# Kernel optimization log

Hardware: AMD Instinct MI355X
Metric: run time of the kernel (lower is better)

Reference implementation:

```python
import jax, jax.numpy as jnp
import numpy as np

N, E, IN, H, D = 100000, 1600000, 128, 4, 64
NEG_SLOPE = 0.2
K_APPNP, ALPHA = 5, 0.5
BN_EPS = 1e-5


def setup_inputs() -> dict:
    key = jax.random.key(0)
    ks = jax.random.split(key, 12)
    return {
        'node_feats': jax.random.normal(ks[0], (N, IN), jnp.float32),
        'src': jax.random.randint(ks[1], (E,), 0, N, jnp.int32),
        'dst': jax.random.randint(ks[2], (E,), 0, N, jnp.int32),
        'W_fc': jax.random.normal(ks[3], (IN, H * D), jnp.float32) * (1.0 / np.sqrt(IN)),
        'attn_l': jax.random.normal(ks[4], (H, D), jnp.float32) * 0.1,
        'attn_r': jax.random.normal(ks[5], (H, D), jnp.float32) * 0.1,
        'W_res_gat': jax.random.normal(ks[6], (IN, H * D), jnp.float32) * (1.0 / np.sqrt(IN)),
        'gat_bias': jax.random.normal(ks[7], (H * D,), jnp.float32) * 0.01,
        'conv_w': jax.random.normal(ks[8], (1, H), jnp.float32) * 0.5,
        'conv_b': jax.random.normal(ks[9], (1,), jnp.float32) * 0.01,
        'W_res': jax.random.normal(ks[10], (D, IN), jnp.float32) * (1.0 / np.sqrt(IN)),
        'b_res': jax.random.normal(ks[11], (D,), jnp.float32) * 0.01,
        'gamma': jnp.ones((D,), jnp.float32),
        'beta': jnp.zeros((D,), jnp.float32),
    }


def reference(node_feats, src, dst, W_fc, attn_l, attn_r, W_res_gat, gat_bias,
              conv_w, conv_b, W_res, b_res, gamma, beta):
    # ---- GATConv (4 heads, residual, relu) ----
    feat = (node_feats @ W_fc).reshape(N, H, D)            # (N,H,D)
    el = jnp.einsum('nhd,hd->nh', feat, attn_l)            # (N,H)
    er = jnp.einsum('nhd,hd->nh', feat, attn_r)
    e = jax.nn.leaky_relu(el[src] + er[dst], NEG_SLOPE)    # (E,H)
    # edge softmax over incoming edges of each dst node
    emax = jax.ops.segment_max(e, dst, num_segments=N)     # (N,H)
    emax = jnp.where(jnp.isfinite(emax), emax, 0.0)
    ee = jnp.exp(e - emax[dst])                            # (E,H)
    denom = jax.ops.segment_sum(ee, dst, num_segments=N)   # (N,H)
    a = ee / jnp.maximum(denom[dst], 1e-9)                 # (E,H)
    msg = feat[src] * a[..., None]                         # (E,H,D)
    rst = jax.ops.segment_sum(msg, dst, num_segments=N)    # (N,H,D)
    resval = (node_feats @ W_res_gat).reshape(N, H, D)
    rst = jax.nn.relu(rst + resval + gat_bias.reshape(1, H, D))
    # ---- Conv1d (heads -> 1, kernel_size=1) then flatten ----
    h = jnp.einsum('nhd,oh->nod', rst, conv_w) + conv_b[None, :, None]
    h = h.reshape(N, D)
    # ---- APPNP (k=5, alpha=0.5), symmetric deg^{-1/2} norm (in-degree, clamp 1) ----
    deg = jax.ops.segment_sum(jnp.ones((E,), jnp.float32), dst, num_segments=N)
    norm = jnp.power(jnp.maximum(deg, 1.0), -0.5)[:, None]  # (N,1)
    h0 = h
    for _ in range(K_APPNP):
        h = jax.ops.segment_sum((h * norm)[src], dst, num_segments=N) * norm
        h = (1.0 - ALPHA) * h + ALPHA * h0
    # ---- residual linear + relu ----
    h = h + jax.nn.relu(node_feats @ W_res.T + b_res)
    # ---- BatchNorm1d (batch stats, affine) ----
    mu = h.mean(axis=0)
    var = h.var(axis=0)
    return (h - mu) * jax.lax.rsqrt(var + BN_EPS) * gamma + beta
```

## Files before the change

kernel.cpp:

```cpp
#include <hip/hip_runtime.h>
#include <math.h>

#define NN 100000
#define NE 1600000
#define NEG_SLOPE 0.2f
#define GB 98
#define GP 6250
#define SCR 2411u

typedef __attribute__((ext_vector_type(8))) short bf16x8;
typedef __attribute__((ext_vector_type(4))) float f32x4;
typedef __attribute__((ext_vector_type(2))) float f32x2;

__device__ __forceinline__ float b2f(unsigned short u) {
  union { unsigned u; float f; } c; c.u = ((unsigned)u) << 16; return c.f;
}
__device__ __forceinline__ unsigned short f2b(float x) {
  union { float f; unsigned u; } c; c.f = x;
  unsigned r = c.u + 0x7FFFu + ((c.u >> 16) & 1u);
  return (unsigned short)(r >> 16);
}
__device__ __forceinline__ void fma4(float4& acc, float s, const float4& b) {
  acc.x = fmaf(s, b.x, acc.x);
  acc.y = fmaf(s, b.y, acc.y);
  acc.z = fmaf(s, b.z, acc.z);
  acc.w = fmaf(s, b.w, acc.w);
}

__global__ __launch_bounds__(256) void k_zero(int* __restrict__ p, int nwords) {
  int i = blockIdx.x * 256 + threadIdx.x;
  if (i < nwords) p[i] = 0;
}

__global__ void k_zrow(unsigned short* __restrict__ a, unsigned short* __restrict__ b,
                       unsigned short* __restrict__ c) {
  int i = threadIdx.x;
  a[(size_t)NN * 64 + i] = 0;
  b[(size_t)NN * 64 + i] = 0;
  c[(size_t)NN * 64 + i] = 0;
}

__global__ __launch_bounds__(256) void k_cast(const float* __restrict__ A, unsigned short* __restrict__ Ab) {
  int i = blockIdx.x * 256 + threadIdx.x;
  int i4 = i * 4;
  if (i4 < NN * 128) {
    float4 v = *(const float4*)&A[i4];
    ushort4 o; o.x = f2b(v.x); o.y = f2b(v.y); o.z = f2b(v.z); o.w = f2b(v.w);
    *(ushort4*)&Ab[i4] = o;
  }
}

__global__ __launch_bounds__(256) void k_deg(const int* __restrict__ dst, int* __restrict__ deg) {
  int i = blockIdx.x * 256 + threadIdx.x;
  if (i < NE) atomicAdd(&deg[dst[i]], 1);
}

__global__ __launch_bounds__(256) void k_hist(const int* __restrict__ deg, int* __restrict__ bcount,
                                              int* __restrict__ bsum) {
  __shared__ int hist[64];
  __shared__ int red[256];
  int tid = threadIdx.x, blk = blockIdx.x;
  if (tid < 64) hist[tid] = 0;
  __syncthreads();
  int i0 = blk * 1024 + tid * 4;
  int s = 0;
#pragma unroll
  for (int r = 0; r < 4; ++r) {
    int i = i0 + r;
    if (i < NN) {
      int d = deg[i];
      s += d;
      atomicAdd(&hist[d < 63 ? d : 63], 1);
    }
  }
  red[tid] = s;
  __syncthreads();
  if (tid < 128) red[tid] += red[tid + 128];
  __syncthreads();
  if (tid < 64) {
    int v = red[tid] + red[tid + 64];
#pragma unroll
    for (int off = 32; off > 0; off >>= 1) v += __shfl_xor(v, off, 64);
    if (tid == 0) bsum[blk] = v;
    bcount[blk * 64 + tid] = hist[tid];
  }
}

__global__ void k_scan(int* __restrict__ bcount, const int* __restrict__ bsum,
                       int* __restrict__ dbase, int* __restrict__ bbase) {
  __shared__ int tot[64];
  int tid = threadIdx.x;
  {
    int s = 0;
#pragma unroll 7
    for (int blk = 0; blk < GB; ++blk) {
      int v = bcount[blk * 64 + tid];
      bcount[blk * 64 + tid] = s;
      s += v;
    }
    tot[tid] = s;
  }
  __syncthreads();
  if (tid == 0) {
    int base = 0;
    for (int b = 0; b < 64; ++b) { dbase[b] = base; base += tot[b]; }
  }
  if (tid == 1) {
    int s = 0;
#pragma unroll 7
    for (int blk = 0; blk < GB; ++blk) { bbase[blk] = s; s += bsum[blk]; }
  }
}

__global__ __launch_bounds__(256) void k_rows(const int* __restrict__ deg, const int* __restrict__ bcount,
                                              const int* __restrict__ dbase, const int* __restrict__ bbase,
                                              int* __restrict__ row_start, float* __restrict__ nrm,
                                              int* __restrict__ perm) {
  __shared__ int hist[64];
  __shared__ int sc[256];
  int tid = threadIdx.x, blk = blockIdx.x;
  if (tid < 64) hist[tid] = 0;
  int i0 = blk * 1024 + tid * 4;
  int d[4];
#pragma unroll
  for (int r = 0; r < 4; ++r) d[r] = (i0 + r < NN) ? deg[i0 + r] : 0;
  int ts = d[0] + d[1] + d[2] + d[3];
  sc[tid] = ts;
  __syncthreads();
  for (int off = 1; off < 256; off <<= 1) {
    int v = (tid >= off) ? sc[tid - off] : 0;
    __syncthreads();
    sc[tid] += v;
    __syncthreads();
  }
  int base = bbase[blk] + sc[tid] - ts;
#pragma unroll
  for (int r = 0; r < 4; ++r) {
    int i = i0 + r;
    if (i < NN) {
      row_start[i] = base;
      nrm[i] = rsqrtf(fmaxf((float)d[r], 1.0f));
      base += d[r];
      int b = d[r] < 63 ? d[r] : 63;
      int rank = atomicAdd(&hist[b], 1);
      perm[dbase[b] + bcount[blk * 64 + b] + rank] = i;
    }
  }
}

__global__ __launch_bounds__(256) void k_scatter(const int* __restrict__ src, const int* __restrict__ dst,
                                                 const int* __restrict__ row_start, int* __restrict__ cursor,
                                                 int* __restrict__ csr_src) {
  int i = blockIdx.x * 256 + threadIdx.x;
  if (i < NE) {
    int n = dst[i];
    int p = atomicAdd(&cursor[n], 1);
    csr_src[row_start[n] + p] = src[i];
  }
}

__global__ __launch_bounds__(256) void k_prepw(const float* __restrict__ W_fc, const float* __restrict__ al,
                                               const float* __restrict__ ar, float* __restrict__ w) {
  int o = blockIdx.x * 256 + threadIdx.x;
  if (o >= 1024) return;
  int side = o >> 9;
  int h = (o >> 7) & 3;
  int k = o & 127;
  const float* a = side ? ar : al;
  float s = 0.f;
  for (int d = 0; d < 64; ++d) s += W_fc[k * 256 + h * 64 + d] * a[h * 64 + d];
  w[(side * 4 + h) * 128 + k] = s;
}

__global__ __launch_bounds__(256) void k_elr2(const unsigned short* __restrict__ X, const float* __restrict__ w,
                                              float* __restrict__ el, float* __restrict__ er) {
  int n = blockIdx.x * 32 + (threadIdx.x >> 3);
  int p = threadIdx.x & 7;
  if (n >= NN) return;
  const uint4* xr = (const uint4*)(X + (size_t)n * 128);
  const float4* wr = (const float4*)(w + p * 128);
  float s = 0.f;
#pragma unroll
  for (int i = 0; i < 16; ++i) {
    uint4 x = xr[i];
    float4 w0 = wr[2 * i], w1 = wr[2 * i + 1];
    s += __uint_as_float(x.x << 16) * w0.x + __uint_as_float(x.x & 0xFFFF0000u) * w0.y
       + __uint_as_float(x.y << 16) * w0.z + __uint_as_float(x.y & 0xFFFF0000u) * w0.w
       + __uint_as_float(x.z << 16) * w1.x + __uint_as_float(x.z & 0xFFFF0000u) * w1.y
       + __uint_as_float(x.w << 16) * w1.z + __uint_as_float(x.w & 0xFFFF0000u) * w1.w;
  }
  if (p < 4) el[n * 4 + p] = s;
  else er[n * 4 + (p - 4)] = s;
}

__global__ __launch_bounds__(256) void k_prepB(const float* __restrict__ W_fc, const float* __restrict__ W_rg,
                                               unsigned short* __restrict__ Bp) {
  int y = blockIdx.y;
  const float* Bsrc = (y >> 1) ? W_rg : W_fc;
  int colbase = (y & 1) * 128;
  for (int e = blockIdx.x * 256 + threadIdx.x; e < 16384; e += 2048) {
    int n = e & 127, k = e >> 7;
    int p = colbase + n;
    int d = p >> 2, hh = p & 3;
    float v = Bsrc[k * 256 + hh * 64 + d];
    int nt = n >> 4, nn = n & 15, kt = k >> 5, quad = (k >> 3) & 3, j = k & 7;
    Bp[(size_t)y * 16384 + ((kt * 8 + nt) * 64 + quad * 16 + nn) * 8 + j] = f2b(v);
  }
}

__global__ __launch_bounds__(256) void k_gemm_mfma(const unsigned short* __restrict__ Abf,
                                                   const unsigned short* __restrict__ Bp,
                                                   unsigned* __restrict__ feat8u,
                                                   unsigned short* __restrict__ resval2) {
  __shared__ unsigned short Al[128 * 136];
  __shared__ unsigned short Bl[8192];
  int tid = threadIdx.x;
  int half = blockIdx.y >> 1;
  int colbase = (blockIdx.y & 1) * 128;
  int row0 = blockIdx.x * 128;
#pragma unroll
  for (int i = 0; i < 8; ++i) {
    int c = tid + i * 256;
    int row = c >> 4, part = c & 15;
    int gr = row0 + row; if (gr > NN - 1) gr = NN - 1;
    *(uint4*)&Al[row * 136 + part * 8] = *(const uint4*)&Abf[(size_t)gr * 128 + part * 8];
  }
  {
    const uint4* srcb = (const uint4*)(Bp + (size_t)blockIdx.y * 16384);
    uint4* dst4 = (uint4*)Bl;
#pragma unroll
    for (int i = 0; i < 4; ++i) dst4[tid + i * 256] = srcb[tid + i * 256];
  }
  __syncthreads();
  int w = tid >> 6, lane = tid & 63;
  int quad = lane >> 4, l16 = lane & 15;
  f32x4 acc[8][2];
#pragma unroll
  for (int rt = 0; rt < 8; ++rt)
#pragma unroll
    for (int c = 0; c < 2; ++c) acc[rt][c] = (f32x4){0.f, 0.f, 0.f, 0.f};
#pragma unroll
  for (int kh = 0; kh < 2; ++kh) {
    if (kh == 1) {
      __syncthreads();
      const uint4* srcb = (const uint4*)(Bp + (size_t)blockIdx.y * 16384 + 8192);
      uint4* dst4 = (uint4*)Bl;
#pragma unroll
      for (int i = 0; i < 4; ++i) dst4[tid + i * 256] = srcb[tid + i * 256];
      __syncthreads();
    }
#pragma unroll
    for (int ktl = 0; ktl < 2; ++ktl) {
      int kt = kh * 2 + ktl;
      bf16x8 b0 = *(const bf16x8*)&Bl[((ktl * 8 + w * 2 + 0) * 64 + lane) * 8];
      bf16x8 b1 = *(const bf16x8*)&Bl[((ktl * 8 + w * 2 + 1) * 64 + lane) * 8];
      int kb = kt * 32 + quad * 8;
#pragma unroll
      for (int rt = 0; rt < 8; ++rt) {
        bf16x8 a = *(const bf16x8*)&Al[(rt * 16 + l16) * 136 + kb];
        acc[rt][0] = __builtin_amdgcn_mfma_f32_16x16x32_bf16(b0, a, acc[rt][0], 0, 0, 0);
        acc[rt][1] = __builtin_amdgcn_mfma_f32_16x16x32_bf16(b1, a, acc[rt][1], 0, 0, 0);
      }
    }
  }
  __syncthreads();
  if (half == 0) {
    unsigned* Cl = (unsigned*)Al;
#pragma unroll
    for (int rt = 0; rt < 8; ++rt)
#pragma unroll
      for (int c = 0; c < 2; ++c) {
        int pk = __builtin_amdgcn_cvt_pk_fp8_f32(acc[rt][c][0], acc[rt][c][1], 0, false);
        pk = __builtin_amdgcn_cvt_pk_fp8_f32(acc[rt][c][2], acc[rt][c][3], pk, true);
        Cl[(rt * 16 + l16) * 36 + (w * 2 + c) * 4 + quad] = (unsigned)pk;
      }
    __syncthreads();
#pragma unroll
    for (int i = 0; i < 4; ++i) {
      int c = tid + i * 256;
      int row = c >> 3, wp = c & 7;
      int m = row0 + row;
      if (m < NN)
        *(uint4*)&feat8u[(size_t)m * 64 + (colbase >> 2) + wp * 4] = *(const uint4*)&Cl[row * 36 + wp * 4];
    }
  } else {
#pragma unroll
    for (int rt = 0; rt < 8; ++rt)
#pragma unroll
      for (int c = 0; c < 2; ++c) {
        int col = (w * 2 + c) * 16 + quad * 4;
        ushort4 o;
        o.x = f2b(acc[rt][c][0]); o.y = f2b(acc[rt][c][1]);
        o.z = f2b(acc[rt][c][2]); o.w = f2b(acc[rt][c][3]);
        *(ushort4*)&Al[(rt * 16 + l16) * 136 + col] = o;
      }
    __syncthreads();
#pragma unroll
    for (int i = 0; i < 8; ++i) {
      int c = tid + i * 256;
      int row = c >> 4, part = c & 15;
      int m = row0 + row;
      if (m < NN)
        *(uint4*)&resval2[(size_t)m * 256 + colbase + part * 8] = *(const uint4*)&Al[row * 136 + part * 8];
    }
  }
}

__global__ __launch_bounds__(256) void k_gemm_nt_bias_relu(const float* __restrict__ A, const float* __restrict__ B,
                                                           const float* __restrict__ bias, float* __restrict__ C) {
  __shared__ float Bl[128][68];
  for (int idx = threadIdx.x; idx < 64 * 128; idx += 256) {
    int d = idx >> 7, k = idx & 127;
    Bl[k][d] = B[d * 128 + k];
  }
  __syncthreads();
  int tx = threadIdx.x & 15, ty = threadIdx.x >> 4;
  int row0 = blockIdx.x * 64 + ty * 4;
  const float* ap[4];
#pragma unroll
  for (int r = 0; r < 4; ++r) ap[r] = A + (size_t)min(row0 + r, NN - 1) * 128;
  float4 acc[4];
#pragma unroll
  for (int r = 0; r < 4; ++r) acc[r] = make_float4(0.f, 0.f, 0.f, 0.f);
#pragma unroll 2
  for (int k0 = 0; k0 < 128; k0 += 4) {
    float4 b0 = *(const float4*)&Bl[k0][tx * 4];
    float4 b1 = *(const float4*)&Bl[k0 + 1][tx * 4];
    float4 b2 = *(const float4*)&Bl[k0 + 2][tx * 4];
    float4 b3 = *(const float4*)&Bl[k0 + 3][tx * 4];
#pragma unroll
    for (int r = 0; r < 4; ++r) {
      float4 a = *(const float4*)(ap[r] + k0);
      fma4(acc[r], a.x, b0); fma4(acc[r], a.y, b1);
      fma4(acc[r], a.z, b2); fma4(acc[r], a.w, b3);
    }
  }
  float4 bv = *(const float4*)&bias[tx * 4];
#pragma unroll
  for (int r = 0; r < 4; ++r) {
    int row = row0 + r;
    if (row < NN) {
      float4 v;
      v.x = fmaxf(acc[r].x + bv.x, 0.f);
      v.y = fmaxf(acc[r].y + bv.y, 0.f);
      v.z = fmaxf(acc[r].z + bv.z, 0.f);
      v.w = fmaxf(acc[r].w + bv.w, 0.f);
      *(float4*)&C[(size_t)row * 64 + tx * 4] = v;
    }
  }
}

__global__ __launch_bounds__(256) void k_gat(const int* __restrict__ perm, const int* __restrict__ row_start,
                                             const int* __restrict__ deg, const int* __restrict__ csr_src,
                                             const float* __restrict__ el, const float* __restrict__ er,
                                             const unsigned* __restrict__ feat8u,
                                             const unsigned short* __restrict__ resval2,
                                             const float* __restrict__ gat_bias, const float* __restrict__ conv_w,
                                             const float* __restrict__ conv_b, const float* __restrict__ nrm,
                                             float* __restrict__ h0, unsigned short* __restrict__ hs0o) {
  __shared__ int s_src[4][16][4];
  __shared__ float s_x[4][16][4][4];
  int wid = threadIdx.x >> 6, lane = threadIdx.x & 63;
  int g = lane >> 4, k = lane & 15;
  int chunk = (int)(((unsigned)blockIdx.x * SCR) % (unsigned)GP);
  int n = perm[chunk * 16 + wid * 4 + g];
  int s0 = row_start[n], cnt = deg[n];
  float4 er4 = *(const float4*)&er[n * 4];
  unsigned koff = (unsigned)(k << 4);
  f32x2 a01[4], a23[4];
#pragma unroll
  for (int i = 0; i < 4; ++i) { a01[i] = (f32x2){0.f, 0.f}; a23[i] = (f32x2){0.f, 0.f}; }
  f32x2 den01 = (f32x2){0.f, 0.f}, den23 = (f32x2){0.f, 0.f};
  int cm = cnt;
  cm = max(cm, __shfl_xor(cm, 16, 64));
  cm = max(cm, __shfl_xor(cm, 32, 64));
  for (int base = 0; base < cm; base += 16) {
    int j = base + k;
    int s = 0;
    float x0 = 0.f, x1 = 0.f, x2 = 0.f, x3 = 0.f;
    if (j < cnt) {
      s = csr_src[s0 + j];
      float4 el4 = *(const float4*)&el[s * 4];
      float e0 = el4.x + er4.x; e0 = (e0 > 0.f) ? e0 : NEG_SLOPE * e0;
      float e1 = el4.y + er4.y; e1 = (e1 > 0.f) ? e1 : NEG_SLOPE * e1;
      float e2 = el4.z + er4.z; e2 = (e2 > 0.f) ? e2 : NEG_SLOPE * e2;
      float e3 = el4.w + er4.w; e3 = (e3 > 0.f) ? e3 : NEG_SLOPE * e3;
      x0 = __expf(e0); x1 = __expf(e1); x2 = __expf(e2); x3 = __expf(e3);
      den01 += (f32x2){x0, x1}; den23 += (f32x2){x2, x3};
    }
    s_src[wid][k][g] = s;
    *(float4*)&s_x[wid][k][g][0] = make_float4(x0, x1, x2, x3);
    int tm = cm - base; if (tm > 16) tm = 16;
    int tm2 = (tm + 1) & ~1;
    for (int t = 0; t < tm2; t += 2) {
      int sa = s_src[wid][t][g];
      int sb = s_src[wid][t + 1][g];
      uint4 fa = *(const uint4*)((const char*)feat8u + (((unsigned)sa << 8) + koff));
      uint4 fb = *(const uint4*)((const char*)feat8u + (((unsigned)sb << 8) + koff));
      float4 xa = *(const float4*)&s_x[wid][t][g][0];
      float4 xb = *(const float4*)&s_x[wid][t + 1][g][0];
      {
        f32x2 x01 = (f32x2){xa.x, xa.y}, x23 = (f32x2){xa.z, xa.w};
        f32x2 lo, hi;
        lo = __builtin_amdgcn_cvt_pk_f32_fp8((int)fa.x, false);
        hi = __builtin_amdgcn_cvt_pk_f32_fp8((int)fa.x, true);
        a01[0] += x01 * lo; a23[0] += x23 * hi;
        lo = __builtin_amdgcn_cvt_pk_f32_fp8((int)fa.y, false);
        hi = __builtin_amdgcn_cvt_pk_f32_fp8((int)fa.y, true);
        a01[1] += x01 * lo; a23[1] += x23 * hi;
        lo = __builtin_amdgcn_cvt_pk_f32_fp8((int)fa.z, false);
        hi = __builtin_amdgcn_cvt_pk_f32_fp8((int)fa.z, true);
        a01[2] += x01 * lo; a23[2] += x23 * hi;
        lo = __builtin_amdgcn_cvt_pk_f32_fp8((int)fa.w, false);
        hi = __builtin_amdgcn_cvt_pk_f32_fp8((int)fa.w, true);
        a01[3] += x01 * lo; a23[3] += x23 * hi;
      }
      {
        f32x2 x01 = (f32x2){xb.x, xb.y}, x23 = (f32x2){xb.z, xb.w};
        f32x2 lo, hi;
        lo = __builtin_amdgcn_cvt_pk_f32_fp8((int)fb.x, false);
        hi = __builtin_amdgcn_cvt_pk_f32_fp8((int)fb.x, true);
        a01[0] += x01 * lo; a23[0] += x23 * hi;
        lo = __builtin_amdgcn_cvt_pk_f32_fp8((int)fb.y, false);
        hi = __builtin_amdgcn_cvt_pk_f32_fp8((int)fb.y, true);
        a01[1] += x01 * lo; a23[1] += x23 * hi;
        lo = __builtin_amdgcn_cvt_pk_f32_fp8((int)fb.z, false);
        hi = __builtin_amdgcn_cvt_pk_f32_fp8((int)fb.z, true);
        a01[2] += x01 * lo; a23[2] += x23 * hi;
        lo = __builtin_amdgcn_cvt_pk_f32_fp8((int)fb.w, false);
        hi = __builtin_amdgcn_cvt_pk_f32_fp8((int)fb.w, true);
        a01[3] += x01 * lo; a23[3] += x23 * hi;
      }
    }
  }
#pragma unroll
  for (int off = 1; off < 16; off <<= 1) {
    den01[0] += __shfl_xor(den01[0], off, 64);
    den01[1] += __shfl_xor(den01[1], off, 64);
    den23[0] += __shfl_xor(den23[0], off, 64);
    den23[1] += __shfl_xor(den23[1], off, 64);
  }
  float i0 = 1.f / fmaxf(den01[0], 1e-9f);
  float i1 = 1.f / fmaxf(den01[1], 1e-9f);
  float i2 = 1.f / fmaxf(den23[0], 1e-9f);
  float i3 = 1.f / fmaxf(den23[1], 1e-9f);
  uint4 rv0 = *(const uint4*)&resval2[(size_t)n * 256 + (k << 4)];
  uint4 rv1 = *(const uint4*)&resval2[(size_t)n * 256 + (k << 4) + 8];
  unsigned short c[16];
  *(uint4*)&c[0] = rv0; *(uint4*)&c[8] = rv1;
  int d0 = k << 2;
  float4 b0 = *(const float4*)&gat_bias[d0];
  float4 b1 = *(const float4*)&gat_bias[64 + d0];
  float4 b2 = *(const float4*)&gat_bias[128 + d0];
  float4 b3 = *(const float4*)&gat_bias[192 + d0];
  float bh0[4] = {b0.x, b0.y, b0.z, b0.w};
  float bh1[4] = {b1.x, b1.y, b1.z, b1.w};
  float bh2[4] = {b2.x, b2.y, b2.z, b2.w};
  float bh3[4] = {b3.x, b3.y, b3.z, b3.w};
  float cb = conv_b[0];
  float cw0 = conv_w[0], cw1 = conv_w[1], cw2 = conv_w[2], cw3 = conv_w[3];
  float hm[4];
#pragma unroll
  for (int i = 0; i < 4; ++i) {
    float t_, hmv = cb;
    t_ = fmaf(a01[i][0], i0, b2f(c[4 * i + 0]) + bh0[i]); t_ = fmaxf(t_, 0.f); hmv = fmaf(cw0, t_, hmv);
    t_ = fmaf(a01[i][1], i1, b2f(c[4 * i + 1]) + bh1[i]); t_ = fmaxf(t_, 0.f); hmv = fmaf(cw1, t_, hmv);
    t_ = fmaf(a23[i][0], i2, b2f(c[4 * i + 2]) + bh2[i]); t_ = fmaxf(t_, 0.f); hmv = fmaf(cw2, t_, hmv);
    t_ = fmaf(a23[i][1], i3, b2f(c[4 * i + 3]) + bh3[i]); t_ = fmaxf(t_, 0.f); hmv = fmaf(cw3, t_, hmv);
    hm[i] = hmv;
  }
  float nn_ = nrm[n];
  size_t o = (size_t)n * 64 + d0;
  *(float4*)&h0[o] = make_float4(hm[0], hm[1], hm[2], hm[3]);
  ushort4 hs;
  hs.x = f2b(hm[0] * nn_); hs.y = f2b(hm[1] * nn_);
  hs.z = f2b(hm[2] * nn_); hs.w = f2b(hm[3] * nn_);
  *(ushort4*)&hs0o[o] = hs;
}

__device__ __forceinline__ void gather4(const int* __restrict__ perm, const int* __restrict__ row_start,
                                        const int* __restrict__ deg, const int* __restrict__ csr_src,
                                        const unsigned short* __restrict__ hs_in,
                                        int wid, int lane, int& n, int& k, float (&a)[4]) {
  __shared__ int s_src[4][16][4];
  int g = lane >> 4; k = lane & 15;
  int chunk = (int)(((unsigned)blockIdx.x * SCR) % (unsigned)GP);
  n = perm[chunk * 16 + wid * 4 + g];
  int s0 = row_start[n], cnt = deg[n];
  unsigned koff = (unsigned)(k << 3);
  a[0] = 0.f; a[1] = 0.f; a[2] = 0.f; a[3] = 0.f;
  int cm = cnt;
  cm = max(cm, __shfl_xor(cm, 16, 64));
  cm = max(cm, __shfl_xor(cm, 32, 64));
  for (int base = 0; base < cm; base += 16) {
    int j = base + k;
    s_src[wid][k][g] = (j < cnt) ? csr_src[s0 + j] : NN;
    int tm = cm - base; if (tm > 16) tm = 16;
    int tm4 = (tm + 3) & ~3;
    for (int t = 0; t < tm4; t += 4) {
      int sa = s_src[wid][t][g];
      int sb = s_src[wid][t + 1][g];
      int sc2 = s_src[wid][t + 2][g];
      int sd = s_src[wid][t + 3][g];
      uint2 ua = *(const uint2*)((const char*)hs_in + (((unsigned)sa << 7) + koff));
      uint2 ub = *(const uint2*)((const char*)hs_in + (((unsigned)sb << 7) + koff));
      uint2 uc = *(const uint2*)((const char*)hs_in + (((unsigned)sc2 << 7) + koff));
      uint2 ud = *(const uint2*)((const char*)hs_in + (((unsigned)sd << 7) + koff));
      a[0] += __uint_as_float(ua.x << 16) + __uint_as_float(ub.x << 16);
      a[1] += __uint_as_float(ua.x & 0xFFFF0000u) + __uint_as_float(ub.x & 0xFFFF0000u);
      a[2] += __uint_as_float(ua.y << 16) + __uint_as_float(ub.y << 16);
      a[3] += __uint_as_float(ua.y & 0xFFFF0000u) + __uint_as_float(ub.y & 0xFFFF0000u);
      a[0] += __uint_as_float(uc.x << 16) + __uint_as_float(ud.x << 16);
      a[1] += __uint_as_float(uc.x & 0xFFFF0000u) + __uint_as_float(ud.x & 0xFFFF0000u);
      a[2] += __uint_as_float(uc.y << 16) + __uint_as_float(ud.y << 16);
      a[3] += __uint_as_float(uc.y & 0xFFFF0000u) + __uint_as_float(ud.y & 0xFFFF0000u);
    }
  }
}

__global__ __launch_bounds__(256) void k_gather_mid(const int* __restrict__ perm, const int* __restrict__ row_start,
                                                    const int* __restrict__ deg, const int* __restrict__ csr_src,
                                                    const unsigned short* __restrict__ hs_in,
                                                    const float* __restrict__ nrm,
                                                    const unsigned short* __restrict__ hs0,
                                                    unsigned short* __restrict__ hs_out) {
  int wid = threadIdx.x >> 6, lane = threadIdx.x & 63;
  int n, k; float a[4];
  gather4(perm, row_start, deg, csr_src, hs_in, wid, lane, n, k, a);
  size_t o = (size_t)n * 64 + (k << 2);
  float nn_ = nrm[n];
  float hnn = 0.5f * nn_ * nn_;
  uint2 z = *(const uint2*)&hs0[o];
  ushort4 ov;
  ov.x = f2b(fmaf(hnn, a[0], 0.5f * __uint_as_float(z.x << 16)));
  ov.y = f2b(fmaf(hnn, a[1], 0.5f * __uint_as_float(z.x & 0xFFFF0000u)));
  ov.z = f2b(fmaf(hnn, a[2], 0.5f * __uint_as_float(z.y << 16)));
  ov.w = f2b(fmaf(hnn, a[3], 0.5f * __uint_as_float(z.y & 0xFFFF0000u)));
  *(ushort4*)&hs_out[o] = ov;
}

__global__ __launch_bounds__(256) void k_gather_last(const int* __restrict__ perm, const int* __restrict__ row_start,
                                                     const int* __restrict__ deg, const int* __restrict__ csr_src,
                                                     const unsigned short* __restrict__ hs_in,
                                                     const float* __restrict__ nrm,
                                                     const float* __restrict__ res2,
                                                     float* h0io) {
  int wid = threadIdx.x >> 6, lane = threadIdx.x & 63;
  int n, k; float a[4];
  gather4(perm, row_start, deg, csr_src, hs_in, wid, lane, n, k, a);
  size_t o = (size_t)n * 64 + (k << 2);
  float nn_ = nrm[n];
  float hn = 0.5f * nn_;
  float4 h4 = *(const float4*)&h0io[o];
  float4 r4 = *(const float4*)&res2[o];
  float4 v;
  v.x = fmaf(hn, a[0], 0.5f * h4.x) + r4.x;
  v.y = fmaf(hn, a[1], 0.5f * h4.y) + r4.y;
  v.z = fmaf(hn, a[2], 0.5f * h4.z) + r4.z;
  v.w = fmaf(hn, a[3], 0.5f * h4.w) + r4.w;
  *(float4*)&h0io[o] = v;
}

__global__ __launch_bounds__(256) void k_finred(const float* __restrict__ hfin, float* __restrict__ bn) {
  __shared__ float s1[256], s2[256];
  int d = threadIdx.x & 63;
  int rb = blockIdx.x * 64;
  float sum = 0.f, sq = 0.f;
  for (int r = threadIdx.x >> 6; r < 64; r += 4) {
    int n = rb + r;
    if (n < NN) {
      float v = hfin[(size_t)n * 64 + d];
      sum += v; sq += v * v;
    }
  }
  s1[threadIdx.x] = sum; s2[threadIdx.x] = sq;
  __syncthreads();
  if (threadIdx.x < 128) { s1[threadIdx.x] += s1[threadIdx.x + 128]; s2[threadIdx.x] += s2[threadIdx.x + 128]; }
  __syncthreads();
  if (threadIdx.x < 64) {
    atomicAdd(&bn[d], s1[threadIdx.x] + s1[threadIdx.x + 64]);
    atomicAdd(&bn[64 + d], s2[threadIdx.x] + s2[threadIdx.x + 64]);
  }
}

__global__ void k_bnstats(const float* __restrict__ bn, const float* __restrict__ gamma,
                          const float* __restrict__ beta, float* __restrict__ bns) {
  int d = threadIdx.x;
  float mu = bn[d] * (1.0f / NN);
  float var = fmaxf(bn[64 + d] * (1.0f / NN) - mu * mu, 0.f);
  float sc = rsqrtf(var + 1e-5f) * gamma[d];
  bns[d] = sc;
  bns[64 + d] = beta[d] - mu * sc;
}

__global__ __launch_bounds__(256) void k_bnapply(const float* __restrict__ h, const float* __restrict__ bns,
                                                 float* __restrict__ out) {
  int i = blockIdx.x * 256 + threadIdx.x;
  if (i < NN * 64) {
    int d = i & 63;
    out[i] = fmaf(h[i], bns[d], bns[64 + d]);
  }
}

extern "C" void kernel_launch(void* const* d_in, const int* in_sizes, int n_in,
                              void* d_out, int out_size, void* d_ws, size_t ws_size,
                              hipStream_t stream) {
  const float* node_feats = (const float*)d_in[0];
  const int* src = (const int*)d_in[1];
  const int* dst = (const int*)d_in[2];
  const float* W_fc = (const float*)d_in[3];
  const float* attn_l = (const float*)d_in[4];
  const float* attn_r = (const float*)d_in[5];
  const float* W_res_gat = (const float*)d_in[6];
  const float* gat_bias = (const float*)d_in[7];
  const float* conv_w = (const float*)d_in[8];
  const float* conv_b = (const float*)d_in[9];
  const float* W_res = (const float*)d_in[10];
  const float* b_res = (const float*)d_in[11];
  const float* gamma = (const float*)d_in[12];
  const float* beta = (const float*)d_in[13];
  float* out = (float*)d_out;

  char* base = (char*)d_ws;
  size_t off = 0;
  auto alloc = [&](size_t bytes) -> char* {
    char* p = base + off;
    off = (off + bytes + 255) & ~(size_t)255;
    return p;
  };
  unsigned* feat8u        = (unsigned*)alloc((size_t)NN * 256);
  unsigned short* resval2 = (unsigned short*)alloc((size_t)NN * 256 * 2);
  float* res2             = (float*)resval2;
  float* el               = (float*)alloc((size_t)NN * 4 * 4);
  float* er               = (float*)alloc((size_t)NN * 4 * 4);
  float* h0               = (float*)alloc((size_t)NN * 64 * 4);
  unsigned short* Abf     = (unsigned short*)h0;
  unsigned short* hs0     = (unsigned short*)alloc((size_t)(NN + 1) * 64 * 2);
  unsigned short* hsA     = (unsigned short*)alloc((size_t)(NN + 1) * 64 * 2);
  unsigned short* hsB     = (unsigned short*)alloc((size_t)(NN + 1) * 64 * 2);
  int* csr_src            = (int*)alloc((size_t)NE * 4);
  float* nrm              = (float*)alloc((size_t)NN * 4);
  int* row_start          = (int*)alloc((size_t)NN * 4);
  int* perm               = (int*)alloc((size_t)NN * 4);
  int* bcount             = (int*)alloc((size_t)GB * 64 * 4);
  int* bsum               = (int*)alloc((size_t)GB * 4);
  int* bbase              = (int*)alloc((size_t)GB * 4);
  int* dbase              = (int*)alloc(64 * 4);
  unsigned short* Bpacked = (unsigned short*)alloc((size_t)4 * 16384 * 2);
  float* w_elr            = (float*)alloc((size_t)8 * 128 * 4);
  size_t zoff = off;
  int* deg                = (int*)alloc((size_t)NN * 4);
  int* cursor             = (int*)alloc((size_t)NN * 4);
  float* bn               = (float*)alloc(256 * 4);
  float* hfin             = h0;

  int zwords = (int)((off - zoff) / 4);
  int gE = (NE + 255) / 256;
  int gM = (NN + 63) / 64;
  int gV = (NN * 64 + 255) / 256;

  k_zero<<<(zwords + 255) / 256, 256, 0, stream>>>((int*)(base + zoff), zwords);
  k_zrow<<<1, 64, 0, stream>>>(hs0, hsA, hsB);
  k_deg<<<gE, 256, 0, stream>>>(dst, deg);
  k_hist<<<GB, 256, 0, stream>>>(deg, bcount, bsum);
  k_scan<<<1, 64, 0, stream>>>(bcount, bsum, dbase, bbase);
  k_rows<<<GB, 256, 0, stream>>>(deg, bcount, dbase, bbase, row_start, nrm, perm);
  k_scatter<<<gE, 256, 0, stream>>>(src, dst, row_start, cursor, csr_src);

  k_cast<<<(NN * 128 / 4 + 255) / 256, 256, 0, stream>>>(node_feats, Abf);
  k_prepB<<<dim3(8, 4), 256, 0, stream>>>(W_fc, W_res_gat, Bpacked);
  k_prepw<<<4, 256, 0, stream>>>(W_fc, attn_l, attn_r, w_elr);
  k_gemm_mfma<<<dim3((NN + 127) / 128, 4), 256, 0, stream>>>(Abf, Bpacked, feat8u, resval2);

  k_elr2<<<(NN + 31) / 32, 256, 0, stream>>>(Abf, w_elr, el, er);
  k_gat<<<GP, 256, 0, stream>>>(perm, row_start, deg, csr_src, el, er, feat8u, resval2,
                                gat_bias, conv_w, conv_b, nrm, h0, hs0);

  k_gemm_nt_bias_relu<<<gM, 256, 0, stream>>>(node_feats, W_res, b_res, res2);

  k_gather_mid<<<GP, 256, 0, stream>>>(perm, row_start, deg, csr_src, hs0, nrm, hs0, hsA);
  k_gather_mid<<<GP, 256, 0, stream>>>(perm, row_start, deg, csr_src, hsA, nrm, hs0, hsB);
  k_gather_mid<<<GP, 256, 0, stream>>>(perm, row_start, deg, csr_src, hsB, nrm, hs0, hsA);
  k_gather_mid<<<GP, 256, 0, stream>>>(perm, row_start, deg, csr_src, hsA, nrm, hs0, hsB);
  k_gather_last<<<GP, 256, 0, stream>>>(perm, row_start, deg, csr_src, hsB, nrm, res2, hfin);

  k_finred<<<gM, 256, 0, stream>>>(hfin, bn);
  k_bnstats<<<1, 64, 0, stream>>>(bn, gamma, beta, bn + 128);
  k_bnapply<<<gV, 256, 0, stream>>>(hfin, bn + 128, out);
}
```

Baseline: 729.0 us.

## Slice APPNP feature table into 8 column planes to shrink gather working set

Stores the bf16 scaled node features as 8 separate column slices of 16 bytes per node. Each APPNP block now handles one slice for 128 nodes, with two lanes per node, so each pass gathers from a table about 1.6MB in size that fits in cache. The GAT kernel no longer writes the fp32 h0. The last APPNP step instead rebuilds h0 from the bf16 scaled copy by dividing out the norm, which avoids one fp32 read and write but adds bf16 rounding error to h0. The trade-off is 8x more blocks, each re-reading CSR indices and degrees, and serial per-edge loads with less memory-level parallelism.

```diff
diff --git a/kernel.cpp b/kernel.cpp
--- a/kernel.cpp
+++ b/kernel.cpp
@@ -7,6 +7,9 @@
 #define GB 98
 #define GP 6250
 #define SCR 2411u
+#define NCH 782
+#define SCR2 389u
+#define SST ((NN + 1) * 8)
 
 typedef __attribute__((ext_vector_type(8))) short bf16x8;
 typedef __attribute__((ext_vector_type(4))) float f32x4;
@@ -35,9 +38,8 @@
 __global__ void k_zrow(unsigned short* __restrict__ a, unsigned short* __restrict__ b,
                        unsigned short* __restrict__ c) {
   int i = threadIdx.x;
-  a[(size_t)NN * 64 + i] = 0;
-  b[(size_t)NN * 64 + i] = 0;
-  c[(size_t)NN * 64 + i] = 0;
+  int idx = (i >> 3) * SST + NN * 8 + (i & 7);
+  a[idx] = 0; b[idx] = 0; c[idx] = 0;
 }
 
 __global__ __launch_bounds__(256) void k_cast(const float* __restrict__ A, unsigned short* __restrict__ Ab) {
@@ -357,7 +359,7 @@
                                              const unsigned short* __restrict__ resval2,
                                              const float* __restrict__ gat_bias, const float* __restrict__ conv_w,
                                              const float* __restrict__ conv_b, const float* __restrict__ nrm,
-                                             float* __restrict__ h0, unsigned short* __restrict__ hs0o) {
+                                             unsigned short* __restrict__ hs0o) {
   __shared__ int s_src[4][16][4];
   __shared__ float s_x[4][16][4][4];
   int wid = threadIdx.x >> 6, lane = threadIdx.x & 63;
@@ -470,95 +472,95 @@
     hm[i] = hmv;
   }
   float nn_ = nrm[n];
-  size_t o = (size_t)n * 64 + d0;
-  *(float4*)&h0[o] = make_float4(hm[0], hm[1], hm[2], hm[3]);
   ushort4 hs;
   hs.x = f2b(hm[0] * nn_); hs.y = f2b(hm[1] * nn_);
   hs.z = f2b(hm[2] * nn_); hs.w = f2b(hm[3] * nn_);
-  *(ushort4*)&hs0o[o] = hs;
-}
-
-__device__ __forceinline__ void gather4(const int* __restrict__ perm, const int* __restrict__ row_start,
-                                        const int* __restrict__ deg, const int* __restrict__ csr_src,
-                                        const unsigned short* __restrict__ hs_in,
-                                        int wid, int lane, int& n, int& k, float (&a)[4]) {
-  __shared__ int s_src[4][16][4];
-  int g = lane >> 4; k = lane & 15;
-  int chunk = (int)(((unsigned)blockIdx.x * SCR) % (unsigned)GP);
-  n = perm[chunk * 16 + wid * 4 + g];
-  int s0 = row_start[n], cnt = deg[n];
-  unsigned koff = (unsigned)(k << 3);
+  *(ushort4*)&hs0o[(size_t)(k >> 1) * SST + n * 8 + ((k & 1) << 2)] = hs;
+}
+
+__device__ __forceinline__ void appnp_core(const int* __restrict__ perm, const int* __restrict__ row_start,
+                                           const int* __restrict__ deg, const int* __restrict__ csr_src,
+                                           const unsigned short* __restrict__ hs_in,
+                                           int& s, int& n, int& h, bool& valid, float (&a)[4]) {
+  __shared__ int s_src[4][16][32];
+  int tid = threadIdx.x;
+  int wid = tid >> 6, lane = tid & 63;
+  int m = lane >> 1; h = lane & 1;
+  s = blockIdx.x & 7;
+  int chunk = (int)((((unsigned)blockIdx.x >> 3) * SCR2) % (unsigned)NCH);
+  int idx = chunk * 128 + wid * 32 + m;
+  valid = idx < NN;
+  n = perm[valid ? idx : NN - 1];
+  int cnt = valid ? deg[n] : 0;
+  int s0 = row_start[n];
+  const char* tbl = (const char*)(hs_in + (size_t)s * SST);
   a[0] = 0.f; a[1] = 0.f; a[2] = 0.f; a[3] = 0.f;
   int cm = cnt;
-  cm = max(cm, __shfl_xor(cm, 16, 64));
-  cm = max(cm, __shfl_xor(cm, 32, 64));
+#pragma unroll
+  for (int off = 1; off < 64; off <<= 1) cm = max(cm, __shfl_xor(cm, off, 64));
   for (int base = 0; base < cm; base += 16) {
-    int j = base + k;
-    s_src[wid][k][g] = (j < cnt) ? csr_src[s0 + j] : NN;
+#pragma unroll
+    for (int q = 0; q < 8; ++q) {
+      int slot = h * 8 + q;
+      int j = base + slot;
+      s_src[wid][slot][m] = (j < cnt) ? csr_src[s0 + j] : NN;
+    }
     int tm = cm - base; if (tm > 16) tm = 16;
-    int tm4 = (tm + 3) & ~3;
-    for (int t = 0; t < tm4; t += 4) {
-      int sa = s_src[wid][t][g];
-      int sb = s_src[wid][t + 1][g];
-      int sc2 = s_src[wid][t + 2][g];
-      int sd = s_src[wid][t + 3][g];
-      uint2 ua = *(const uint2*)((const char*)hs_in + (((unsigned)sa << 7) + koff));
-      uint2 ub = *(const uint2*)((const char*)hs_in + (((unsigned)sb << 7) + koff));
-      uint2 uc = *(const uint2*)((const char*)hs_in + (((unsigned)sc2 << 7) + koff));
-      uint2 ud = *(const uint2*)((const char*)hs_in + (((unsigned)sd << 7) + koff));
-      a[0] += __uint_as_float(ua.x << 16) + __uint_as_float(ub.x << 16);
-      a[1] += __uint_as_float(ua.x & 0xFFFF0000u) + __uint_as_float(ub.x & 0xFFFF0000u);
-      a[2] += __uint_as_float(ua.y << 16) + __uint_as_float(ub.y << 16);
-      a[3] += __uint_as_float(ua.y & 0xFFFF0000u) + __uint_as_float(ub.y & 0xFFFF0000u);
-      a[0] += __uint_as_float(uc.x << 16) + __uint_as_float(ud.x << 16);
-      a[1] += __uint_as_float(uc.x & 0xFFFF0000u) + __uint_as_float(ud.x & 0xFFFF0000u);
-      a[2] += __uint_as_float(uc.y << 16) + __uint_as_float(ud.y << 16);
-      a[3] += __uint_as_float(uc.y & 0xFFFF0000u) + __uint_as_float(ud.y & 0xFFFF0000u);
-    }
-  }
-}
-
-__global__ __launch_bounds__(256) void k_gather_mid(const int* __restrict__ perm, const int* __restrict__ row_start,
+    for (int t = 0; t < tm; ++t) {
+      int sidx = s_src[wid][t][m];
+      uint2 u = *(const uint2*)(tbl + (((unsigned)sidx << 4) + (h << 3)));
+      a[0] += __uint_as_float(u.x << 16);
+      a[1] += __uint_as_float(u.x & 0xFFFF0000u);
+      a[2] += __uint_as_float(u.y << 16);
+      a[3] += __uint_as_float(u.y & 0xFFFF0000u);
+    }
+  }
+}
+
+__global__ __launch_bounds__(256) void k_appnp_mid(const int* __restrict__ perm, const int* __restrict__ row_start,
+                                                   const int* __restrict__ deg, const int* __restrict__ csr_src,
+                                                   const unsigned short* __restrict__ hs_in,
+                                                   const float* __restrict__ nrm,
+                                                   const unsigned short* __restrict__ hs0,
+                                                   unsigned short* __restrict__ hs_out) {
+  int s, n, h; bool valid; float a[4];
+  appnp_core(perm, row_start, deg, csr_src, hs_in, s, n, h, valid, a);
+  if (valid) {
+    float nn_ = nrm[n];
+    float hnn = 0.5f * nn_ * nn_;
+    uint2 z = *(const uint2*)((const char*)(hs0 + (size_t)s * SST) + ((n << 4) + (h << 3)));
+    ushort4 ov;
+    ov.x = f2b(fmaf(hnn, a[0], 0.5f * __uint_as_float(z.x << 16)));
+    ov.y = f2b(fmaf(hnn, a[1], 0.5f * __uint_as_float(z.x & 0xFFFF0000u)));
+    ov.z = f2b(fmaf(hnn, a[2], 0.5f * __uint_as_float(z.y << 16)));
+    ov.w = f2b(fmaf(hnn, a[3], 0.5f * __uint_as_float(z.y & 0xFFFF0000u)));
+    *(ushort4*)&hs_out[(size_t)s * SST + n * 8 + (h << 2)] = ov;
+  }
+}
+
+__global__ __launch_bounds__(256) void k_appnp_last(const int* __restrict__ perm, const int* __restrict__ row_start,
                                                     const int* __restrict__ deg, const int* __restrict__ csr_src,
                                                     const unsigned short* __restrict__ hs_in,
                                                     const float* __restrict__ nrm,
                                                     const unsigned short* __restrict__ hs0,
-                                                    unsigned short* __restrict__ hs_out) {
-  int wid = threadIdx.x >> 6, lane = threadIdx.x & 63;
-  int n, k; float a[4];
-  gather4(perm, row_start, deg, csr_src, hs_in, wid, lane, n, k, a);
-  size_t o = (size_t)n * 64 + (k << 2);
-  float nn_ = nrm[n];
-  float hnn = 0.5f * nn_ * nn_;
-  uint2 z = *(const uint2*)&hs0[o];
-  ushort4 ov;
-  ov.x = f2b(fmaf(hnn, a[0], 0.5f * __uint_as_float(z.x << 16)));
-  ov.y = f2b(fmaf(hnn, a[1], 0.5f * __uint_as_float(z.x & 0xFFFF0000u)));
-  ov.z = f2b(fmaf(hnn, a[2], 0.5f * __uint_as_float(z.y << 16)));
-  ov.w = f2b(fmaf(hnn, a[3], 0.5f * __uint_as_float(z.y & 0xFFFF0000u)));
-  *(ushort4*)&hs_out[o] = ov;
-}
-
-__global__ __launch_bounds__(256) void k_gather_last(const int* __restrict__ perm, const int* __restrict__ row_start,
-                                                     const int* __restrict__ deg, const int* __restrict__ csr_src,
-                                                     const unsigned short* __restrict__ hs_in,
-                                                     const float* __restrict__ nrm,
-                                                     const float* __restrict__ res2,
-                                                     float* h0io) {
-  int wid = threadIdx.x >> 6, lane = threadIdx.x & 63;
-  int n, k; float a[4];
-  gather4(perm, row_start, deg, csr_src, hs_in, wid, lane, n, k, a);
-  size_t o = (size_t)n * 64 + (k << 2);
-  float nn_ = nrm[n];
-  float hn = 0.5f * nn_;
-  float4 h4 = *(const float4*)&h0io[o];
-  float4 r4 = *(const float4*)&res2[o];
-  float4 v;
-  v.x = fmaf(hn, a[0], 0.5f * h4.x) + r4.x;
-  v.y = fmaf(hn, a[1], 0.5f * h4.y) + r4.y;
-  v.z = fmaf(hn, a[2], 0.5f * h4.z) + r4.z;
-  v.w = fmaf(hn, a[3], 0.5f * h4.w) + r4.w;
-  *(float4*)&h0io[o] = v;
+                                                    const float* __restrict__ res2,
+                                                    float* __restrict__ hfin) {
+  int s, n, h; bool valid; float a[4];
+  appnp_core(perm, row_start, deg, csr_src, hs_in, s, n, h, valid, a);
+  if (valid) {
+    float nn_ = nrm[n];
+    float hn = 0.5f * nn_;
+    float hi = 0.5f / nn_;
+    uint2 z = *(const uint2*)((const char*)(hs0 + (size_t)s * SST) + ((n << 4) + (h << 3)));
+    size_t o = (size_t)n * 64 + s * 8 + (h << 2);
+    float4 r4 = *(const float4*)&res2[o];
+    float4 v;
+    v.x = fmaf(hn, a[0], hi * __uint_as_float(z.x << 16)) + r4.x;
+    v.y = fmaf(hn, a[1], hi * __uint_as_float(z.x & 0xFFFF0000u)) + r4.y;
+    v.z = fmaf(hn, a[2], hi * __uint_as_float(z.y << 16)) + r4.z;
+    v.w = fmaf(hn, a[3], hi * __uint_as_float(z.y & 0xFFFF0000u)) + r4.w;
+    *(float4*)&hfin[o] = v;
+  }
 }
 
 __global__ __launch_bounds__(256) void k_finred(const float* __restrict__ hfin, float* __restrict__ bn) {
@@ -658,6 +660,7 @@
   int gE = (NE + 255) / 256;
   int gM = (NN + 63) / 64;
   int gV = (NN * 64 + 255) / 256;
+  int gAP = 8 * NCH;
 
   k_zero<<<(zwords + 255) / 256, 256, 0, stream>>>((int*)(base + zoff), zwords);
   k_zrow<<<1, 64, 0, stream>>>(hs0, hsA, hsB);
@@ -674,15 +677,15 @@
 
   k_elr2<<<(NN + 31) / 32, 256, 0, stream>>>(Abf, w_elr, el, er);
   k_gat<<<GP, 256, 0, stream>>>(perm, row_start, deg, csr_src, el, er, feat8u, resval2,
-                                gat_bias, conv_w, conv_b, nrm, h0, hs0);
+                                gat_bias, conv_w, conv_b, nrm, hs0);
 
   k_gemm_nt_bias_relu<<<gM, 256, 0, stream>>>(node_feats, W_res, b_res, res2);
 
-  k_gather_mid<<<GP, 256, 0, stream>>>(perm, row_start, deg, csr_src, hs0, nrm, hs0, hsA);
-  k_gather_mid<<<GP, 256, 0, stream>>>(perm, row_start, deg, csr_src, hsA, nrm, hs0, hsB);
-  k_gather_mid<<<GP, 256, 0, stream>>>(perm, row_start, deg, csr_src, hsB, nrm, hs0, hsA);
-  k_gather_mid<<<GP, 256, 0, stream>>>(perm, row_start, deg, csr_src, hsA, nrm, hs0, hsB);
-  k_gather_last<<<GP, 256, 0, stream>>>(perm, row_start, deg, csr_src, hsB, nrm, res2, hfin);
+  k_appnp_mid<<<gAP, 256, 0, stream>>>(perm, row_start, deg, csr_src, hs0, nrm, hs0, hsA);
+  k_appnp_mid<<<gAP, 256, 0, stream>>>(perm, row_start, deg, csr_src, hsA, nrm, hs0, hsB);
+  k_appnp_mid<<<gAP, 256, 0, stream>>>(perm, row_start, deg, csr_src, hsB, nrm, hs0, hsA);
+  k_appnp_mid<<<gAP, 256, 0, stream>>>(perm, row_start, deg, csr_src, hsA, nrm, hs0, hsB);
+  k_appnp_last<<<gAP, 256, 0, stream>>>(perm, row_start, deg, csr_src, hsB, nrm, hs0, res2, hfin);
 
   k_finred<<<gM, 256, 0, stream>>>(hfin, bn);
   k_bnstats<<<1, 64, 0, stream>>>(bn, gamma, beta, bn + 128);
```

After: 1.189 ms. 1.63x slower.
